# Kernel tuning notes

Measured on AMD Instinct MI355X. Metric: run time of the kernel, lower is better.

Reference implementation:

```python
import jax, jax.numpy as jnp
import numpy as np

B, L1, L2, C = 8, 2048, 2048, 320
H, D = 8, 64            # heads, dim_head -> inner_dim = 512
NREG = 4                # num_register_tokens
INNER = H * D
SCALE = D ** -0.5


def setup_inputs() -> dict:
    key = jax.random.key(0)
    ks = jax.random.split(key, 9)
    x = jax.random.normal(ks[0], (B, L1, C), dtype=jnp.float32)
    context = jax.random.normal(ks[1], (B, L2, C), dtype=jnp.float32)
    attn_mask = jax.random.randint(ks[2], (B, L1, L2), 0, 2).astype(bool)
    s = C ** -0.5
    Wq = jax.random.normal(ks[3], (C, INNER), dtype=jnp.float32) * s
    Wk = jax.random.normal(ks[4], (C, INNER), dtype=jnp.float32) * s
    Wv = jax.random.normal(ks[5], (C, INNER), dtype=jnp.float32) * s
    Wo = jax.random.normal(ks[6], (INNER, C), dtype=jnp.float32) * (INNER ** -0.5)
    bo = jnp.zeros((C,), dtype=jnp.float32)
    reg_tokens = jax.random.normal(ks[7], (1, NREG, C), dtype=jnp.float32)
    return {"x": x, "context": context, "attn_mask": attn_mask,
            "Wq": Wq, "Wk": Wk, "Wv": Wv, "Wo": Wo, "bo": bo,
            "reg_tokens": reg_tokens}


def reference(x, context, attn_mask, Wq, Wk, Wv, Wo, bo, reg_tokens):
    b = x.shape[0]
    # prepend register tokens to context: [B, NREG+L2, C]
    ctx = jnp.concatenate([jnp.broadcast_to(reg_tokens, (b, NREG, C)), context], axis=1)
    q = (x @ Wq).reshape(b, L1, H, D).transpose(0, 2, 1, 3)          # B H L1 D
    k = (ctx @ Wk).reshape(b, NREG + L2, H, D).transpose(0, 2, 1, 3)  # B H Lk D
    v = (ctx @ Wv).reshape(b, NREG + L2, H, D).transpose(0, 2, 1, 3)
    # pad mask with True for register tokens (always visible)
    mask = jnp.pad(attn_mask, ((0, 0), (0, 0), (NREG, 0)), constant_values=True)
    scores = jnp.einsum('bhqd,bhkd->bhqk', q, k) * SCALE              # B H L1 Lk
    scores = jnp.where(mask[:, None, :, :], scores, -jnp.inf)
    attn = jax.nn.softmax(scores, axis=-1)
    out = jnp.einsum('bhqk,bhkd->bhqd', attn, v)                      # B H L1 D
    out = out.transpose(0, 2, 1, 3).reshape(b, L1, INNER)             # B L1 (H D)
    return out @ Wo + bo
```

## Files before the change

kernel.cpp:

```cpp
#include <hip/hip_runtime.h>
#include <hip/hip_bf16.h>

#define B_ 8
#define L1_ 2048
#define L2_ 2048
#define C_ 320
#define H_ 8
#define D_ 64
#define NREG_ 4
#define INNER_ 512
#define LK_ 2052
#define LKP_ 2112
#define NKV_TILES 33
#define LOG2E 1.44269504f
#define QSCALE (0.125f * LOG2E)


typedef __bf16 bf16_t;
typedef __attribute__((ext_vector_type(8))) __bf16 bf16x8;
typedef __attribute__((ext_vector_type(4))) __bf16 bf16x4;
typedef __attribute__((ext_vector_type(4))) float f32x4;
typedef __attribute__((ext_vector_type(4))) unsigned int u32x4;

__device__ __forceinline__ f32x4 mfma16(bf16x8 a, bf16x8 b, f32x4 c){
  return __builtin_amdgcn_mfma_f32_16x16x32_bf16(a, b, c, 0, 0, 0);
}

__device__ __forceinline__ void gl_lds16(const char* g, char* l){
  __builtin_amdgcn_global_load_lds(
      (const __attribute__((address_space(1))) unsigned int*)g,
      (__attribute__((address_space(3))) unsigned int*)l, 16, 0, 0);
}

__device__ __forceinline__ float fexp2(float x){
  float r; asm("v_exp_f32 %0, %1" : "=v"(r) : "v"(x)); return r;
}

__device__ __forceinline__ unsigned cvtpk(float a, float b){
  unsigned r; asm("v_cvt_pk_bf16_f32 %0, %1, %2" : "=v"(r) : "v"(a), "v"(b)); return r;
}

__device__ __forceinline__ unsigned byte2bits(unsigned u){
  unsigned b = 0;
  b |= (u & 0x000000FFu) ? 1u : 0u;
  b |= (u & 0x0000FF00u) ? 2u : 0u;
  b |= (u & 0x00FF0000u) ? 4u : 0u;
  b |= (u & 0xFF000000u) ? 8u : 0u;
  return b;
}

__device__ __forceinline__ int swzK(int row){ return (row & 3) | ((row >> 1) & 4); }
__device__ __forceinline__ int swzV(int row){ return row & 7; }

__global__ __launch_bounds__(256)
void k_prep(const float* __restrict__ Wq, const float* __restrict__ Wk,
            const float* __restrict__ Wv, const float* __restrict__ Wo,
            bf16_t* __restrict__ Wqt, bf16_t* __restrict__ Wkt,
            bf16_t* __restrict__ Wvt, bf16_t* __restrict__ Wot,
            const float* __restrict__ x, const float* __restrict__ ctx,
            const float* __restrict__ regt,
            bf16_t* __restrict__ xb, bf16_t* __restrict__ ctxb,
            const void* __restrict__ maskv, unsigned int* __restrict__ maskp)
{
  int bid = blockIdx.x;
  int tid = threadIdx.x;
  if (bid < 1024){
    int z = bid >> 8, r = bid & 255, bx = r & 15, by = r >> 4;
    int K = (z < 3) ? C_ : INNER_;
    int N = (z < 3) ? INNER_ : C_;
    if (bx * 32 >= N || by * 32 >= K) return;
    const float* W = (z == 0) ? Wq : (z == 1) ? Wk : (z == 2) ? Wv : Wo;
    bf16_t* Wt = (z == 0) ? Wqt : (z == 1) ? Wkt : (z == 2) ? Wvt : Wot;
    float sc = (z == 0) ? QSCALE : 1.0f;
    __shared__ float t[32][33];
    int n0 = bx * 32, k0 = by * 32;
    int tx = tid & 31, ty = tid >> 5;
    for (int rr = ty; rr < 32; rr += 8) t[rr][tx] = W[(long)(k0 + rr) * N + n0 + tx];
    __syncthreads();
    for (int rr = ty; rr < 32; rr += 8) Wt[(long)(n0 + rr) * K + k0 + tx] = (bf16_t)(t[tx][rr] * sc);
  } else if (bid < 11424){
    int b2 = bid - 1024;
    if (b2 < 5120){
      long g = (long)b2 * 256 + tid;
      f32x4 v = *(const f32x4*)(x + g * 4);
      bf16x4 cv;
      cv[0]=(bf16_t)v[0]; cv[1]=(bf16_t)v[1]; cv[2]=(bf16_t)v[2]; cv[3]=(bf16_t)v[3];
      *(bf16x4*)(xb + g * 4) = cv;
    } else {
      long g = (long)(b2 - 5120) * 256 + tid;
      long row = g / 80;
      int col = (int)(g - row * 80) * 4;
      int b = (int)(row / LKP_);
      int rr = (int)(row - (long)b * LKP_);
      f32x4 v = (f32x4){0,0,0,0};
      if (rr < L2_)      v = *(const f32x4*)(ctx + ((long)(b * L1_ + rr)) * C_ + col);
      else if (rr < LK_) v = *(const f32x4*)(regt + (rr - L2_) * C_ + col);
      bf16x4 cv;
      cv[0]=(bf16_t)v[0]; cv[1]=(bf16_t)v[1]; cv[2]=(bf16_t)v[2]; cv[3]=(bf16_t)v[3];
      *(bf16x4*)(ctxb + row * C_ + col) = cv;
    }
  } else {
    int row = (bid - 11424) * 4 + (tid >> 6);
    int l = tid & 63;
    const unsigned char* mb = (const unsigned char*)maskv;
    const int* mi = (const int*)maskv;
    int bad = 0;
    #pragma unroll
    for (int jj = 0; jj < 4; jj++){
      int j = l + jj * 64;
      if ((j & 3) != 0 && mb[j] != 0) bad = 1;
    }
    int isInt = (__ballot(bad) == 0ull) ? 1 : 0;
    unsigned int* orow = maskp + (long)row * 66;
    if (!isInt){
      const unsigned char* rp = mb + (long)row * L2_;
      u32x4 a = *(const u32x4*)(rp + 32 * l);
      u32x4 c = *(const u32x4*)(rp + 32 * l + 16);
      unsigned wdv = 0;
      wdv |= byte2bits(a[0]);
      wdv |= byte2bits(a[1]) << 4;
      wdv |= byte2bits(a[2]) << 8;
      wdv |= byte2bits(a[3]) << 12;
      wdv |= byte2bits(c[0]) << 16;
      wdv |= byte2bits(c[1]) << 20;
      wdv |= byte2bits(c[2]) << 24;
      wdv |= byte2bits(c[3]) << 28;
      orow[l] = wdv;
      if (l == 0) orow[64] = 0x0000000Fu;
      else if (l == 1) orow[65] = 0u;
    } else {
      long base = (long)row * L2_;
      for (int s = 0; s < 33; s++){
        int kv = s * 64 + l;
        int vis;
        if (kv < L2_)      vis = (mi[base + kv] != 0);
        else               vis = (kv < LK_);
        unsigned long long bal = __ballot(vis);
        if (l == 0)      orow[2*s]   = (unsigned int)bal;
        else if (l == 1) orow[2*s+1] = (unsigned int)(bal >> 32);
      }
    }
  }
}

__global__ __launch_bounds__(256)
void k_proj(const bf16_t* __restrict__ xb, const bf16_t* __restrict__ ctxb,
            const bf16_t* __restrict__ Wqt, const bf16_t* __restrict__ Wkt,
            const bf16_t* __restrict__ Wvt,
            bf16_t* __restrict__ Qw, bf16_t* __restrict__ Kw, bf16_t* __restrict__ Vtw)
{
  int lin = blockIdx.x;
  int xcd = lin & 7, idx = lin >> 3;
  int mode, mt_, n_;
  if (idx < 64){
    mode = 0;
    mt_ = xcd * 16 + (idx & 15);
    n_ = idx >> 4;
  } else {
    int j = idx - 64;
    mode = 1 + (j & 1);
    int jj = j >> 1;
    n_ = jj & 3;
    int mm = jj >> 2;
    mt_ = mm * 8 + xcd;
    if (mt_ >= 132) return;
  }
  const char* Ab = (const char*)((mode == 0) ? xb : ctxb);
  const char* Wtb = (const char*)((mode == 0) ? Wqt : (mode == 1) ? Wkt : Wvt);
  bf16_t* out = (mode == 0) ? Qw : (mode == 1) ? Kw : Vtw;

  __shared__ __align__(16) char As[2][128*64*2];
  __shared__ __align__(16) char Bs[2][128*64*2];
  int tid = threadIdx.x;
  int w = tid >> 6, lane = tid & 63, cl = lane & 15, cg = lane >> 4;
  int wr = w >> 1, wc = w & 1;
  int m0 = mt_ * 128, n0 = n_ * 128;

  f32x4 acc[4][4];
  #pragma unroll
  for (int i = 0; i < 4; i++)
    #pragma unroll
    for (int j = 0; j < 4; j++) acc[i][j] = (f32x4){0,0,0,0};

  auto stage = [&](int kb, int buf){
    #pragma unroll
    for (int c = 0; c < 4; c++){
      int e = c * 4096 + tid * 16;
      int row = e >> 7, irb = e & 127;
      gl_lds16(Ab + (long)(m0 + row) * 640 + kb * 128 + (irb ^ ((row & 7) << 4)), As[buf] + e);
    }
    #pragma unroll
    for (int c = 0; c < 4; c++){
      int e = c * 4096 + tid * 16;
      int row = e >> 7, irb = e & 127;
      gl_lds16(Wtb + (long)(n0 + row) * 640 + kb * 128 + (irb ^ ((row & 7) << 4)), Bs[buf] + e);
    }
  };

  stage(0, 0);
  for (int kb = 0; kb < 5; ++kb){
    int buf = kb & 1;
    if (kb < 4){
      stage(kb + 1, buf ^ 1);
      asm volatile("s_waitcnt vmcnt(8)" ::: "memory");
    } else {
      asm volatile("s_waitcnt vmcnt(0)" ::: "memory");
    }
    __syncthreads();
    #pragma unroll
    for (int kc = 0; kc < 2; kc++){
      int kk = kc * 32 + cg * 8;
      bf16x8 af[4], bfr[4];
      #pragma unroll
      for (int mt = 0; mt < 4; mt++){
        int row = wr * 64 + mt * 16 + cl;
        af[mt] = *(const bf16x8*)(As[buf] + (row << 7) + ((kk << 1) ^ ((row & 7) << 4)));
      }
      #pragma unroll
      for (int nt = 0; nt < 4; nt++){
        int row = wc * 64 + nt * 16 + cl;
        bfr[nt] = *(const bf16x8*)(Bs[buf] + (row << 7) + ((kk << 1) ^ ((row & 7) << 4)));
      }
      #pragma unroll
      for (int mt = 0; mt < 4; mt++)
        #pragma unroll
        for (int nt = 0; nt < 4; nt++)
          acc[mt][nt] = mfma16(af[mt], bfr[nt], acc[mt][nt]);
    }
    __syncthreads();
  }

  #pragma unroll
  for (int mt = 0; mt < 4; mt++){
    #pragma unroll
    for (int nt = 0; nt < 4; nt++){
      f32x4 v = acc[mt][nt];
      int row = m0 + wr * 64 + mt * 16 + cg * 4;
      int col = n0 + wc * 64 + nt * 16 + cl;
      int h = col >> 6, d = col & 63;
      if (mode == 0){
        int b = row >> 11, l1 = row & 2047;
        bf16_t* p = out + ((long)((b * H_ + h) * L1_ + l1)) * D_ + d;
        #pragma unroll
        for (int r = 0; r < 4; r++) p[r * D_] = (bf16_t)v[r];
      } else if (mode == 1){
        int b = row / LKP_, rr = row - b * LKP_;
        bf16_t* p = out + ((long)((b * H_ + h) * LKP_ + rr)) * D_ + d;
        #pragma unroll
        for (int r = 0; r < 4; r++) p[r * D_] = (bf16_t)v[r];
      } else {
        int b = row / LKP_, rr = row - b * LKP_;
        bf16x4 cv;
        cv[0]=(bf16_t)v[0]; cv[1]=(bf16_t)v[1]; cv[2]=(bf16_t)v[2]; cv[3]=(bf16_t)v[3];
        *(bf16x4*)(out + ((long)((b * H_ + h) * D_ + d)) * LKP_ + rr) = cv;
      }
    }
  }
}

__global__ __launch_bounds__(512)
void k_attn(const bf16_t* __restrict__ Q, const bf16_t* __restrict__ K,
            const bf16_t* __restrict__ Vt, const unsigned int* __restrict__ maskp,
            bf16_t* __restrict__ att)
{
  __shared__ __align__(16) char smem[33024];
  int lin = blockIdx.x;
  int xcd = lin & 7, idx = lin >> 3;
  int bh = xcd * 8 + (idx >> 3);
  int qb = idx & 7;
  const int b = bh >> 3, h = bh & 7;
  const int tid = threadIdx.x, w = tid >> 6, lane = tid & 63;
  const int cl = lane & 15, cg = lane >> 4;
  const int qw = qb * 256 + w * 32;

  char* lutb = smem + 32768;
  if (tid < 16){
    unsigned n = tid;
    uint2 mk;
    mk.x = ((n & 1u) ? 0x0000FFFFu : 0u) | ((n & 2u) ? 0xFFFF0000u : 0u);
    mk.y = ((n & 4u) ? 0x0000FFFFu : 0u) | ((n & 8u) ? 0xFFFF0000u : 0u);
    *(uint2*)(lutb + tid * 8) = mk;
  }

  const char* Kg = (const char*)(K + (long)bh * LKP_ * D_);
  const char* Vg = (const char*)(Vt + (long)bh * D_ * LKP_);

  bf16x8 qf[2][2];
  const unsigned int* mrow[2];
  #pragma unroll
  for (int qg = 0; qg < 2; qg++){
    const bf16_t* Qb = Q + ((long)bh * L1_ + qw + qg*16 + cl) * D_;
    qf[qg][0] = *(const bf16x8*)(Qb + cg*8);
    qf[qg][1] = *(const bf16x8*)(Qb + 32 + cg*8);
    mrow[qg] = maskp + (long)(b * L1_ + qw + qg*16 + cl) * 66;
  }

  bf16x8 ones8;
  #pragma unroll
  for (int i = 0; i < 8; i++) ones8[i] = (bf16_t)1.0f;

  f32x4 o[2][4];
  f32x4 sacc[2];
  #pragma unroll
  for (int qg = 0; qg < 2; qg++){
    sacc[qg] = (f32x4){0,0,0,0};
    #pragma unroll
    for (int dt = 0; dt < 4; dt++) o[qg][dt] = (f32x4){0,0,0,0};
  }

  const int sp = tid * 16;
  const int srow = sp >> 7, sir = sp & 127;
  const int kgo = (srow << 7) + (sir ^ (swzK(srow) << 4));
  const long vgo = (long)srow * (LKP_ * 2) + (sir ^ (swzV(srow) << 4));

  gl_lds16(Kg + kgo, smem + sp);
  gl_lds16(Vg + vgo, smem + 16384 + sp);
  uint2 wd_cur[2];
  #pragma unroll
  for (int qg = 0; qg < 2; qg++) wd_cur[qg] = *(const uint2*)(mrow[qg]);
  asm volatile("s_waitcnt vmcnt(0)" ::: "memory");
  __syncthreads();

  for (int t = 0; t < NKV_TILES; ++t){
    int tn = (t + 1 < NKV_TILES) ? t + 1 : NKV_TILES - 1;
    gl_lds16(Kg + (long)tn * 8192 + kgo, smem + ((t + 1) & 1) * 8192 + sp);
    gl_lds16(Vg + vgo + tn * 128, smem + 16384 + ((t + 1) & 1) * 8192 + sp);
    uint2 wd_nxt[2];
    #pragma unroll
    for (int qg = 0; qg < 2; qg++) wd_nxt[qg] = *(const uint2*)(mrow[qg] + 2*tn);

    const char* Kb = smem + (t & 1) * 8192;
    const char* Vb = smem + 16384 + (t & 1) * 8192;

    f32x4 s[2][4];
    __builtin_amdgcn_s_setprio(1);
    #pragma unroll
    for (int T = 0; T < 4; T++){
      int row = 32*(T>>1) + 8*(cl>>2) + 4*(T&1) + (cl&3);
      int sw = swzK(row) << 4;
      const char* rp = Kb + (row << 7);
      bf16x8 kf0 = *(const bf16x8*)(rp + ((16*cg) ^ sw));
      bf16x8 kf1 = *(const bf16x8*)(rp + ((64 + 16*cg) ^ sw));
      #pragma unroll
      for (int qg = 0; qg < 2; qg++){
        f32x4 z = (f32x4){0,0,0,0};
        z = mfma16(kf0, qf[qg][0], z);
        z = mfma16(kf1, qf[qg][1], z);
        s[qg][T] = z;
      }
    }
    __builtin_amdgcn_s_setprio(0);

    bf16x8 pa[2][2];
    #pragma unroll
    for (int qg = 0; qg < 2; qg++){
      unsigned wrd[2][4];
      #pragma unroll
      for (int T = 0; T < 4; T++){
        unsigned wsel = (T < 2) ? wd_cur[qg].x : wd_cur[qg].y;
        unsigned nib = (wsel >> (8*cg + 4*(T&1))) & 0xFu;
        uint2 mk = *(const uint2*)(lutb + (nib << 3));
        float p0 = fexp2(s[qg][T][0]);
        float p1 = fexp2(s[qg][T][1]);
        float p2 = fexp2(s[qg][T][2]);
        float p3 = fexp2(s[qg][T][3]);
        unsigned lo = cvtpk(p0, p1) & mk.x;
        unsigned hi = cvtpk(p2, p3) & mk.y;
        wrd[T >> 1][2*(T & 1) + 0] = lo;
        wrd[T >> 1][2*(T & 1) + 1] = hi;
      }
      union { u32x4 u; bf16x8 v; } pk0, pk1;
      pk0.u = (u32x4){wrd[0][0], wrd[0][1], wrd[0][2], wrd[0][3]};
      pk1.u = (u32x4){wrd[1][0], wrd[1][1], wrd[1][2], wrd[1][3]};
      pa[qg][0] = pk0.v;
      pa[qg][1] = pk1.v;
    }

    __builtin_amdgcn_s_setprio(1);
    #pragma unroll
    for (int qg = 0; qg < 2; qg++){
      sacc[qg] = mfma16(ones8, pa[qg][0], sacc[qg]);
      sacc[qg] = mfma16(ones8, pa[qg][1], sacc[qg]);
    }
    #pragma unroll
    for (int dt = 0; dt < 4; dt++){
      int row = 16*dt + cl;
      int sw = swzV(row) << 4;
      const char* rp = Vb + (row << 7);
      bf16x8 vf0 = *(const bf16x8*)(rp + ((16*cg) ^ sw));
      bf16x8 vf1 = *(const bf16x8*)(rp + ((64 + 16*cg) ^ sw));
      #pragma unroll
      for (int qg = 0; qg < 2; qg++){
        o[qg][dt] = mfma16(pa[qg][0], vf0, o[qg][dt]);
        o[qg][dt] = mfma16(pa[qg][1], vf1, o[qg][dt]);
      }
    }
    __builtin_amdgcn_s_setprio(0);

    asm volatile("s_waitcnt vmcnt(0)" ::: "memory");
    __syncthreads();
    wd_cur[0] = wd_nxt[0];
    wd_cur[1] = wd_nxt[1];
  }

  #pragma unroll
  for (int qg = 0; qg < 2; qg++){
    float inv = 1.0f / sacc[qg][0];
    float ir0 = __shfl(inv, (lane & 48) | (cg*4 + 0));
    float ir1 = __shfl(inv, (lane & 48) | (cg*4 + 1));
    float ir2 = __shfl(inv, (lane & 48) | (cg*4 + 2));
    float ir3 = __shfl(inv, (lane & 48) | (cg*4 + 3));
    int qbase = qw + qg*16 + cg*4;
    #pragma unroll
    for (int dt = 0; dt < 4; dt++){
      bf16_t* op = att + ((long)(b * L1_) + qbase) * INNER_ + h * D_ + 16*dt + cl;
      op[0] = (bf16_t)(o[qg][dt][0] * ir0);
      op[INNER_] = (bf16_t)(o[qg][dt][1] * ir1);
      op[2*INNER_] = (bf16_t)(o[qg][dt][2] * ir2);
      op[3*INNER_] = (bf16_t)(o[qg][dt][3] * ir3);
    }
  }
}

__global__ __launch_bounds__(256)
void k_out(const bf16_t* __restrict__ A, const bf16_t* __restrict__ Wot,
           const float* __restrict__ bo, float* __restrict__ out)
{
  __shared__ __align__(16) char As[2][128*64*2];
  __shared__ __align__(16) char Bs[2][64*64*2];
  int lin = blockIdx.x;
  int xcd = lin & 7, idx = lin >> 3;
  int tid = threadIdx.x;
  int w = tid >> 6, lane = tid & 63, cl = lane & 15, cg = lane >> 4;
  int wr = w >> 1, wc = w & 1;
  int m0 = (xcd * 16 + (idx & 15)) * 128, n0 = (idx >> 4) * 64;
  const char* Ab = (const char*)A;
  const char* Bb = (const char*)Wot;

  f32x4 acc[4][2];
  #pragma unroll
  for (int i = 0; i < 4; i++)
    #pragma unroll
    for (int j = 0; j < 2; j++) acc[i][j] = (f32x4){0,0,0,0};

  auto stage = [&](int kb, int buf){
    #pragma unroll
    for (int c = 0; c < 4; c++){
      int e = c * 4096 + tid * 16;
      int row = e >> 7, irb = e & 127;
      gl_lds16(Ab + (long)(m0 + row) * 1024 + kb * 128 + (irb ^ ((row & 7) << 4)), As[buf] + e);
    }
    #pragma unroll
    for (int c = 0; c < 2; c++){
      int e = c * 4096 + tid * 16;
      int row = e >> 7, irb = e & 127;
      gl_lds16(Bb + (long)(n0 + row) * 1024 + kb * 128 + (irb ^ ((row & 7) << 4)), Bs[buf] + e);
    }
  };

  stage(0, 0);
  for (int kb = 0; kb < 8; kb++){
    int buf = kb & 1;
    if (kb < 7){
      stage(kb + 1, buf ^ 1);
      asm volatile("s_waitcnt vmcnt(6)" ::: "memory");
    } else {
      asm volatile("s_waitcnt vmcnt(0)" ::: "memory");
    }
    __syncthreads();
    #pragma unroll
    for (int kc = 0; kc < 2; kc++){
      int kk = kc * 32 + cg * 8;
      bf16x8 af[4], bfr[2];
      #pragma unroll
      for (int mt = 0; mt < 4; mt++){
        int row = wr * 64 + mt * 16 + cl;
        af[mt] = *(const bf16x8*)(As[buf] + (row << 7) + ((kk << 1) ^ ((row & 7) << 4)));
      }
      #pragma unroll
      for (int nt = 0; nt < 2; nt++){
        int row = wc * 32 + nt * 16 + cl;
        bfr[nt] = *(const bf16x8*)(Bs[buf] + (row << 7) + ((kk << 1) ^ ((row & 7) << 4)));
      }
      #pragma unroll
      for (int mt = 0; mt < 4; mt++)
        #pragma unroll
        for (int nt = 0; nt < 2; nt++)
          acc[mt][nt] = mfma16(af[mt], bfr[nt], acc[mt][nt]);
    }
    __syncthreads();
  }
  #pragma unroll
  for (int mt = 0; mt < 4; mt++)
    #pragma unroll
    for (int nt = 0; nt < 2; nt++){
      int row = m0 + wr * 64 + mt * 16 + cg * 4;
      int col = n0 + wc * 32 + nt * 16 + cl;
      float bias = bo[col];
      #pragma unroll
      for (int r = 0; r < 4; r++)
        out[(long)(row + r) * C_ + col] = acc[mt][nt][r] + bias;
    }
}

extern "C" void kernel_launch(void* const* d_in, const int* in_sizes, int n_in,
                              void* d_out, int out_size, void* d_ws, size_t ws_size,
                              hipStream_t stream)
{
  const float* x    = (const float*)d_in[0];
  const float* ctx  = (const float*)d_in[1];
  const void*  mask = d_in[2];
  const float* Wq   = (const float*)d_in[3];
  const float* Wk   = (const float*)d_in[4];
  const float* Wv   = (const float*)d_in[5];
  const float* Wo   = (const float*)d_in[6];
  const float* bo   = (const float*)d_in[7];
  const float* regt = (const float*)d_in[8];
  float* out = (float*)d_out;

  char* ws = (char*)d_ws;
  size_t off = 256;
  unsigned int* maskp = (unsigned int*)(ws + off);    off += (size_t)16384 * 66 * 4;
  bf16_t* Qw  = (bf16_t*)(ws + off);                  off += (size_t)B_*H_*L1_*D_*2;
  bf16_t* Kw  = (bf16_t*)(ws + off);                  off += (size_t)B_*H_*LKP_*D_*2;
  bf16_t* Vtw = (bf16_t*)(ws + off);                  off += (size_t)B_*H_*D_*LKP_*2;
  size_t Roff = off;
  bf16_t* xb   = (bf16_t*)(ws + Roff);
  bf16_t* ctxb = (bf16_t*)(ws + Roff + (size_t)16384*C_*2);
  bf16_t* Att  = (bf16_t*)(ws + Roff);
  off = Roff + (size_t)16384*C_*2 + (size_t)16896*C_*2;
  bf16_t* Wqt = (bf16_t*)(ws + off);                  off += (size_t)C_*INNER_*2;
  bf16_t* Wkt = (bf16_t*)(ws + off);                  off += (size_t)C_*INNER_*2;
  bf16_t* Wvt = (bf16_t*)(ws + off);                  off += (size_t)C_*INNER_*2;
  bf16_t* Wot = (bf16_t*)(ws + off);                  off += (size_t)C_*INNER_*2;
  (void)ws_size; (void)in_sizes; (void)n_in; (void)out_size;

  k_prep<<<15520, 256, 0, stream>>>(Wq, Wk, Wv, Wo, Wqt, Wkt, Wvt, Wot,
                                    x, ctx, regt, xb, ctxb, mask, maskp);
  k_proj<<<1600, 256, 0, stream>>>(xb, ctxb, Wqt, Wkt, Wvt, Qw, Kw, Vtw);
  k_attn<<<512, 512, 0, stream>>>(Qw, Kw, Vtw, maskp, Att);
  k_out<<<640, 256, 0, stream>>>(Att, Wot, bo, out);
}
```

Measured before the change: 179.7 us.

## Move mask bit-packing into projection kernel and widen bf16 conversion stores

Mask bit-packing moves out of the prep kernel and into the projection GEMM kernel. Each projection block runs its GEMM tile (or skips it if out of range) and then packs a grid-strided share of mask rows, so the mask traffic overlaps with the matmul work. The fp32-to-bf16 conversion of x and context now handles two float4 groups per thread with packed conversions and 16-byte stores, which shrinks the prep grid. The risk is that the mask work lengthens some projection blocks and adds tail imbalance, since 1600 blocks cover 4096 row groups unevenly.

```diff
diff --git a/kernel.cpp b/kernel.cpp
--- a/kernel.cpp
+++ b/kernel.cpp
@@ -59,8 +59,7 @@
             bf16_t* __restrict__ Wvt, bf16_t* __restrict__ Wot,
             const float* __restrict__ x, const float* __restrict__ ctx,
             const float* __restrict__ regt,
-            bf16_t* __restrict__ xb, bf16_t* __restrict__ ctxb,
-            const void* __restrict__ maskv, unsigned int* __restrict__ maskp)
+            bf16_t* __restrict__ xb, bf16_t* __restrict__ ctxb)
 {
   int bid = blockIdx.x;
   int tid = threadIdx.x;
@@ -78,16 +77,20 @@
     for (int rr = ty; rr < 32; rr += 8) t[rr][tx] = W[(long)(k0 + rr) * N + n0 + tx];
     __syncthreads();
     for (int rr = ty; rr < 32; rr += 8) Wt[(long)(n0 + rr) * K + k0 + tx] = (bf16_t)(t[tx][rr] * sc);
-  } else if (bid < 11424){
-    int b2 = bid - 1024;
-    if (b2 < 5120){
-      long g = (long)b2 * 256 + tid;
-      f32x4 v = *(const f32x4*)(x + g * 4);
-      bf16x4 cv;
-      cv[0]=(bf16_t)v[0]; cv[1]=(bf16_t)v[1]; cv[2]=(bf16_t)v[2]; cv[3]=(bf16_t)v[3];
-      *(bf16x4*)(xb + g * 4) = cv;
-    } else {
-      long g = (long)(b2 - 5120) * 256 + tid;
+  } else if (bid < 3584){
+    long g0 = ((long)(bid - 1024) * 256 + tid) * 2;
+    f32x4 v0 = *(const f32x4*)(x + g0 * 4);
+    f32x4 v1 = *(const f32x4*)(x + g0 * 4 + 4);
+    union { u32x4 u; bf16x8 v; } pk;
+    pk.u = (u32x4){cvtpk(v0[0], v0[1]), cvtpk(v0[2], v0[3]),
+                   cvtpk(v1[0], v1[1]), cvtpk(v1[2], v1[3])};
+    *(bf16x8*)(xb + g0 * 4) = pk.v;
+  } else {
+    long g0 = ((long)(bid - 3584) * 256 + tid) * 2;
+    f32x4 vv[2];
+    #pragma unroll
+    for (int gg = 0; gg < 2; gg++){
+      long g = g0 + gg;
       long row = g / 80;
       int col = (int)(g - row * 80) * 4;
       int b = (int)(row / LKP_);
@@ -95,51 +98,12 @@
       f32x4 v = (f32x4){0,0,0,0};
       if (rr < L2_)      v = *(const f32x4*)(ctx + ((long)(b * L1_ + rr)) * C_ + col);
       else if (rr < LK_) v = *(const f32x4*)(regt + (rr - L2_) * C_ + col);
-      bf16x4 cv;
-      cv[0]=(bf16_t)v[0]; cv[1]=(bf16_t)v[1]; cv[2]=(bf16_t)v[2]; cv[3]=(bf16_t)v[3];
-      *(bf16x4*)(ctxb + row * C_ + col) = cv;
-    }
-  } else {
-    int row = (bid - 11424) * 4 + (tid >> 6);
-    int l = tid & 63;
-    const unsigned char* mb = (const unsigned char*)maskv;
-    const int* mi = (const int*)maskv;
-    int bad = 0;
-    #pragma unroll
-    for (int jj = 0; jj < 4; jj++){
-      int j = l + jj * 64;
-      if ((j & 3) != 0 && mb[j] != 0) bad = 1;
-    }
-    int isInt = (__ballot(bad) == 0ull) ? 1 : 0;
-    unsigned int* orow = maskp + (long)row * 66;
-    if (!isInt){
-      const unsigned char* rp = mb + (long)row * L2_;
-      u32x4 a = *(const u32x4*)(rp + 32 * l);
-      u32x4 c = *(const u32x4*)(rp + 32 * l + 16);
-      unsigned wdv = 0;
-      wdv |= byte2bits(a[0]);
-      wdv |= byte2bits(a[1]) << 4;
-      wdv |= byte2bits(a[2]) << 8;
-      wdv |= byte2bits(a[3]) << 12;
-      wdv |= byte2bits(c[0]) << 16;
-      wdv |= byte2bits(c[1]) << 20;
-      wdv |= byte2bits(c[2]) << 24;
-      wdv |= byte2bits(c[3]) << 28;
-      orow[l] = wdv;
-      if (l == 0) orow[64] = 0x0000000Fu;
-      else if (l == 1) orow[65] = 0u;
-    } else {
-      long base = (long)row * L2_;
-      for (int s = 0; s < 33; s++){
-        int kv = s * 64 + l;
-        int vis;
-        if (kv < L2_)      vis = (mi[base + kv] != 0);
-        else               vis = (kv < LK_);
-        unsigned long long bal = __ballot(vis);
-        if (l == 0)      orow[2*s]   = (unsigned int)bal;
-        else if (l == 1) orow[2*s+1] = (unsigned int)(bal >> 32);
-      }
-    }
+      vv[gg] = v;
+    }
+    union { u32x4 u; bf16x8 v; } pk;
+    pk.u = (u32x4){cvtpk(vv[0][0], vv[0][1]), cvtpk(vv[0][2], vv[0][3]),
+                   cvtpk(vv[1][0], vv[1][1]), cvtpk(vv[1][2], vv[1][3])};
+    *(bf16x8*)(ctxb + g0 * 4) = pk.v;
   }
 }
 
@@ -147,7 +111,8 @@
 void k_proj(const bf16_t* __restrict__ xb, const bf16_t* __restrict__ ctxb,
             const bf16_t* __restrict__ Wqt, const bf16_t* __restrict__ Wkt,
             const bf16_t* __restrict__ Wvt,
-            bf16_t* __restrict__ Qw, bf16_t* __restrict__ Kw, bf16_t* __restrict__ Vtw)
+            bf16_t* __restrict__ Qw, bf16_t* __restrict__ Kw, bf16_t* __restrict__ Vtw,
+            const void* __restrict__ maskv, unsigned int* __restrict__ maskp)
 {
   int lin = blockIdx.x;
   int xcd = lin & 7, idx = lin >> 3;
@@ -163,96 +128,144 @@
     n_ = jj & 3;
     int mm = jj >> 2;
     mt_ = mm * 8 + xcd;
-    if (mt_ >= 132) return;
-  }
-  const char* Ab = (const char*)((mode == 0) ? xb : ctxb);
-  const char* Wtb = (const char*)((mode == 0) ? Wqt : (mode == 1) ? Wkt : Wvt);
-  bf16_t* out = (mode == 0) ? Qw : (mode == 1) ? Kw : Vtw;
-
-  __shared__ __align__(16) char As[2][128*64*2];
-  __shared__ __align__(16) char Bs[2][128*64*2];
+  }
   int tid = threadIdx.x;
-  int w = tid >> 6, lane = tid & 63, cl = lane & 15, cg = lane >> 4;
-  int wr = w >> 1, wc = w & 1;
-  int m0 = mt_ * 128, n0 = n_ * 128;
-
-  f32x4 acc[4][4];
-  #pragma unroll
-  for (int i = 0; i < 4; i++)
-    #pragma unroll
-    for (int j = 0; j < 4; j++) acc[i][j] = (f32x4){0,0,0,0};
-
-  auto stage = [&](int kb, int buf){
-    #pragma unroll
-    for (int c = 0; c < 4; c++){
-      int e = c * 4096 + tid * 16;
-      int row = e >> 7, irb = e & 127;
-      gl_lds16(Ab + (long)(m0 + row) * 640 + kb * 128 + (irb ^ ((row & 7) << 4)), As[buf] + e);
-    }
-    #pragma unroll
-    for (int c = 0; c < 4; c++){
-      int e = c * 4096 + tid * 16;
-      int row = e >> 7, irb = e & 127;
-      gl_lds16(Wtb + (long)(n0 + row) * 640 + kb * 128 + (irb ^ ((row & 7) << 4)), Bs[buf] + e);
-    }
-  };
-
-  stage(0, 0);
-  for (int kb = 0; kb < 5; ++kb){
-    int buf = kb & 1;
-    if (kb < 4){
-      stage(kb + 1, buf ^ 1);
-      asm volatile("s_waitcnt vmcnt(8)" ::: "memory");
-    } else {
-      asm volatile("s_waitcnt vmcnt(0)" ::: "memory");
-    }
-    __syncthreads();
-    #pragma unroll
-    for (int kc = 0; kc < 2; kc++){
-      int kk = kc * 32 + cg * 8;
-      bf16x8 af[4], bfr[4];
-      #pragma unroll
-      for (int mt = 0; mt < 4; mt++){
-        int row = wr * 64 + mt * 16 + cl;
-        af[mt] = *(const bf16x8*)(As[buf] + (row << 7) + ((kk << 1) ^ ((row & 7) << 4)));
-      }
+  bool valid = (mode == 0) || (mt_ < 132);
+
+  if (valid){
+    const char* Ab = (const char*)((mode == 0) ? xb : ctxb);
+    const char* Wtb = (const char*)((mode == 0) ? Wqt : (mode == 1) ? Wkt : Wvt);
+    bf16_t* out = (mode == 0) ? Qw : (mode == 1) ? Kw : Vtw;
+
+    __shared__ __align__(16) char As[2][128*64*2];
+    __shared__ __align__(16) char Bs[2][128*64*2];
+    int w = tid >> 6, lane = tid & 63, cl = lane & 15, cg = lane >> 4;
+    int wr = w >> 1, wc = w & 1;
+    int m0 = mt_ * 128, n0 = n_ * 128;
+
+    f32x4 acc[4][4];
+    #pragma unroll
+    for (int i = 0; i < 4; i++)
+      #pragma unroll
+      for (int j = 0; j < 4; j++) acc[i][j] = (f32x4){0,0,0,0};
+
+    auto stage = [&](int kb, int buf){
+      #pragma unroll
+      for (int c = 0; c < 4; c++){
+        int e = c * 4096 + tid * 16;
+        int row = e >> 7, irb = e & 127;
+        gl_lds16(Ab + (long)(m0 + row) * 640 + kb * 128 + (irb ^ ((row & 7) << 4)), As[buf] + e);
+      }
+      #pragma unroll
+      for (int c = 0; c < 4; c++){
+        int e = c * 4096 + tid * 16;
+        int row = e >> 7, irb = e & 127;
+        gl_lds16(Wtb + (long)(n0 + row) * 640 + kb * 128 + (irb ^ ((row & 7) << 4)), Bs[buf] + e);
+      }
+    };
+
+    stage(0, 0);
+    for (int kb = 0; kb < 5; ++kb){
+      int buf = kb & 1;
+      if (kb < 4){
+        stage(kb + 1, buf ^ 1);
+        asm volatile("s_waitcnt vmcnt(8)" ::: "memory");
+      } else {
+        asm volatile("s_waitcnt vmcnt(0)" ::: "memory");
+      }
+      __syncthreads();
+      #pragma unroll
+      for (int kc = 0; kc < 2; kc++){
+        int kk = kc * 32 + cg * 8;
+        bf16x8 af[4], bfr[4];
+        #pragma unroll
+        for (int mt = 0; mt < 4; mt++){
+          int row = wr * 64 + mt * 16 + cl;
+          af[mt] = *(const bf16x8*)(As[buf] + (row << 7) + ((kk << 1) ^ ((row & 7) << 4)));
+        }
+        #pragma unroll
+        for (int nt = 0; nt < 4; nt++){
+          int row = wc * 64 + nt * 16 + cl;
+          bfr[nt] = *(const bf16x8*)(Bs[buf] + (row << 7) + ((kk << 1) ^ ((row & 7) << 4)));
+        }
+        #pragma unroll
+        for (int mt = 0; mt < 4; mt++)
+          #pragma unroll
+          for (int nt = 0; nt < 4; nt++)
+            acc[mt][nt] = mfma16(af[mt], bfr[nt], acc[mt][nt]);
+      }
+      __syncthreads();
+    }
+
+    #pragma unroll
+    for (int mt = 0; mt < 4; mt++){
       #pragma unroll
       for (int nt = 0; nt < 4; nt++){
-        int row = wc * 64 + nt * 16 + cl;
-        bfr[nt] = *(const bf16x8*)(Bs[buf] + (row << 7) + ((kk << 1) ^ ((row & 7) << 4)));
-      }
-      #pragma unroll
-      for (int mt = 0; mt < 4; mt++)
-        #pragma unroll
-        for (int nt = 0; nt < 4; nt++)
-          acc[mt][nt] = mfma16(af[mt], bfr[nt], acc[mt][nt]);
-    }
-    __syncthreads();
-  }
-
-  #pragma unroll
-  for (int mt = 0; mt < 4; mt++){
-    #pragma unroll
-    for (int nt = 0; nt < 4; nt++){
-      f32x4 v = acc[mt][nt];
-      int row = m0 + wr * 64 + mt * 16 + cg * 4;
-      int col = n0 + wc * 64 + nt * 16 + cl;
-      int h = col >> 6, d = col & 63;
-      if (mode == 0){
-        int b = row >> 11, l1 = row & 2047;
-        bf16_t* p = out + ((long)((b * H_ + h) * L1_ + l1)) * D_ + d;
-        #pragma unroll
-        for (int r = 0; r < 4; r++) p[r * D_] = (bf16_t)v[r];
-      } else if (mode == 1){
-        int b = row / LKP_, rr = row - b * LKP_;
-        bf16_t* p = out + ((long)((b * H_ + h) * LKP_ + rr)) * D_ + d;
-        #pragma unroll
-        for (int r = 0; r < 4; r++) p[r * D_] = (bf16_t)v[r];
+        f32x4 v = acc[mt][nt];
+        int row = m0 + wr * 64 + mt * 16 + cg * 4;
+        int col = n0 + wc * 64 + nt * 16 + cl;
+        int h = col >> 6, d = col & 63;
+        if (mode == 0){
+          int b = row >> 11, l1 = row & 2047;
+          bf16_t* p = out + ((long)((b * H_ + h) * L1_ + l1)) * D_ + d;
+          #pragma unroll
+          for (int r = 0; r < 4; r++) p[r * D_] = (bf16_t)v[r];
+        } else if (mode == 1){
+          int b = row / LKP_, rr = row - b * LKP_;
+          bf16_t* p = out + ((long)((b * H_ + h) * LKP_ + rr)) * D_ + d;
+          #pragma unroll
+          for (int r = 0; r < 4; r++) p[r * D_] = (bf16_t)v[r];
+        } else {
+          int b = row / LKP_, rr = row - b * LKP_;
+          bf16x4 cv;
+          cv[0]=(bf16_t)v[0]; cv[1]=(bf16_t)v[1]; cv[2]=(bf16_t)v[2]; cv[3]=(bf16_t)v[3];
+          *(bf16x4*)(out + ((long)((b * H_ + h) * D_ + d)) * LKP_ + rr) = cv;
+        }
+      }
+    }
+  }
+
+  {
+    int l = tid & 63;
+    const unsigned char* mb = (const unsigned char*)maskv;
+    const int* mi = (const int*)maskv;
+    int bad = 0;
+    #pragma unroll
+    for (int jj = 0; jj < 4; jj++){
+      int j = l + jj * 64;
+      if ((j & 3) != 0 && mb[j] != 0) bad = 1;
+    }
+    int isInt = (__ballot(bad) == 0ull) ? 1 : 0;
+    for (int mq = lin; mq < 4096; mq += 1600){
+      int row = mq * 4 + (tid >> 6);
+      unsigned int* orow = maskp + (long)row * 66;
+      if (!isInt){
+        const unsigned char* rp = mb + (long)row * L2_;
+        u32x4 a = *(const u32x4*)(rp + 32 * l);
+        u32x4 c = *(const u32x4*)(rp + 32 * l + 16);
+        unsigned wdv = 0;
+        wdv |= byte2bits(a[0]);
+        wdv |= byte2bits(a[1]) << 4;
+        wdv |= byte2bits(a[2]) << 8;
+        wdv |= byte2bits(a[3]) << 12;
+        wdv |= byte2bits(c[0]) << 16;
+        wdv |= byte2bits(c[1]) << 20;
+        wdv |= byte2bits(c[2]) << 24;
+        wdv |= byte2bits(c[3]) << 28;
+        orow[l] = wdv;
+        if (l == 0) orow[64] = 0x0000000Fu;
+        else if (l == 1) orow[65] = 0u;
       } else {
-        int b = row / LKP_, rr = row - b * LKP_;
-        bf16x4 cv;
-        cv[0]=(bf16_t)v[0]; cv[1]=(bf16_t)v[1]; cv[2]=(bf16_t)v[2]; cv[3]=(bf16_t)v[3];
-        *(bf16x4*)(out + ((long)((b * H_ + h) * D_ + d)) * LKP_ + rr) = cv;
+        long base = (long)row * L2_;
+        for (int s = 0; s < 33; s++){
+          int kv = s * 64 + l;
+          int vis;
+          if (kv < L2_) vis = (mi[base + kv] != 0);
+          else          vis = (kv < LK_);
+          unsigned long long bal = __ballot(vis);
+          if (l == 0)      orow[2*s]   = (unsigned int)bal;
+          else if (l == 1) orow[2*s+1] = (unsigned int)(bal >> 32);
+        }
       }
     }
   }
@@ -535,9 +548,9 @@
   bf16_t* Wot = (bf16_t*)(ws + off);                  off += (size_t)C_*INNER_*2;
   (void)ws_size; (void)in_sizes; (void)n_in; (void)out_size;
 
-  k_prep<<<15520, 256, 0, stream>>>(Wq, Wk, Wv, Wo, Wqt, Wkt, Wvt, Wot,
-                                    x, ctx, regt, xb, ctxb, mask, maskp);
-  k_proj<<<1600, 256, 0, stream>>>(xb, ctxb, Wqt, Wkt, Wvt, Qw, Kw, Vtw);
+  k_prep<<<6224, 256, 0, stream>>>(Wq, Wk, Wv, Wo, Wqt, Wkt, Wvt, Wot,
+                                   x, ctx, regt, xb, ctxb);
+  k_proj<<<1600, 256, 0, stream>>>(xb, ctxb, Wqt, Wkt, Wvt, Qw, Kw, Vtw, mask, maskp);
   k_attn<<<512, 512, 0, stream>>>(Qw, Kw, Vtw, maskp, Att);
   k_out<<<640, 256, 0, stream>>>(Att, Wot, bo, out);
 }
```

Result: slower. 270.1 us (+50.3%).

## Fuse fp32-to-bf16 input conversion into projection GEMM operand loads

Applied to the files above, without the earlier changes.

Drops the separate conversion of x and context (plus register tokens) to bf16 from the prep kernel. The projection kernel now reads fp32 activations directly, converts them in registers and writes them into swizzled LDS. This removes a full write and re-read of the bf16 activation copies. In exchange, the projection GEMM loses its double-buffered async pipeline: it becomes single-buffered with synchronous loads, which exposes memory latency. The A-operand global traffic inside the GEMM also doubles because it reads fp32.

```diff
diff --git a/kernel.cpp b/kernel.cpp
--- a/kernel.cpp
+++ b/kernel.cpp
@@ -57,9 +57,6 @@
             const float* __restrict__ Wv, const float* __restrict__ Wo,
             bf16_t* __restrict__ Wqt, bf16_t* __restrict__ Wkt,
             bf16_t* __restrict__ Wvt, bf16_t* __restrict__ Wot,
-            const float* __restrict__ x, const float* __restrict__ ctx,
-            const float* __restrict__ regt,
-            bf16_t* __restrict__ xb, bf16_t* __restrict__ ctxb,
             const void* __restrict__ maskv, unsigned int* __restrict__ maskp)
 {
   int bid = blockIdx.x;
@@ -78,29 +75,8 @@
     for (int rr = ty; rr < 32; rr += 8) t[rr][tx] = W[(long)(k0 + rr) * N + n0 + tx];
     __syncthreads();
     for (int rr = ty; rr < 32; rr += 8) Wt[(long)(n0 + rr) * K + k0 + tx] = (bf16_t)(t[tx][rr] * sc);
-  } else if (bid < 11424){
-    int b2 = bid - 1024;
-    if (b2 < 5120){
-      long g = (long)b2 * 256 + tid;
-      f32x4 v = *(const f32x4*)(x + g * 4);
-      bf16x4 cv;
-      cv[0]=(bf16_t)v[0]; cv[1]=(bf16_t)v[1]; cv[2]=(bf16_t)v[2]; cv[3]=(bf16_t)v[3];
-      *(bf16x4*)(xb + g * 4) = cv;
-    } else {
-      long g = (long)(b2 - 5120) * 256 + tid;
-      long row = g / 80;
-      int col = (int)(g - row * 80) * 4;
-      int b = (int)(row / LKP_);
-      int rr = (int)(row - (long)b * LKP_);
-      f32x4 v = (f32x4){0,0,0,0};
-      if (rr < L2_)      v = *(const f32x4*)(ctx + ((long)(b * L1_ + rr)) * C_ + col);
-      else if (rr < LK_) v = *(const f32x4*)(regt + (rr - L2_) * C_ + col);
-      bf16x4 cv;
-      cv[0]=(bf16_t)v[0]; cv[1]=(bf16_t)v[1]; cv[2]=(bf16_t)v[2]; cv[3]=(bf16_t)v[3];
-      *(bf16x4*)(ctxb + row * C_ + col) = cv;
-    }
   } else {
-    int row = (bid - 11424) * 4 + (tid >> 6);
+    int row = (bid - 1024) * 4 + (tid >> 6);
     int l = tid & 63;
     const unsigned char* mb = (const unsigned char*)maskv;
     const int* mi = (const int*)maskv;
@@ -133,8 +109,8 @@
       for (int s = 0; s < 33; s++){
         int kv = s * 64 + l;
         int vis;
-        if (kv < L2_)      vis = (mi[base + kv] != 0);
-        else               vis = (kv < LK_);
+        if (kv < L2_) vis = (mi[base + kv] != 0);
+        else          vis = (kv < LK_);
         unsigned long long bal = __ballot(vis);
         if (l == 0)      orow[2*s]   = (unsigned int)bal;
         else if (l == 1) orow[2*s+1] = (unsigned int)(bal >> 32);
@@ -144,7 +120,8 @@
 }
 
 __global__ __launch_bounds__(256)
-void k_proj(const bf16_t* __restrict__ xb, const bf16_t* __restrict__ ctxb,
+void k_proj(const float* __restrict__ x, const float* __restrict__ ctx,
+            const float* __restrict__ regt,
             const bf16_t* __restrict__ Wqt, const bf16_t* __restrict__ Wkt,
             const bf16_t* __restrict__ Wvt,
             bf16_t* __restrict__ Qw, bf16_t* __restrict__ Kw, bf16_t* __restrict__ Vtw)
@@ -165,47 +142,63 @@
     mt_ = mm * 8 + xcd;
     if (mt_ >= 132) return;
   }
-  const char* Ab = (const char*)((mode == 0) ? xb : ctxb);
-  const char* Wtb = (const char*)((mode == 0) ? Wqt : (mode == 1) ? Wkt : Wvt);
+  const bf16_t* Wt = (mode == 0) ? Wqt : (mode == 1) ? Wkt : Wvt;
+  const char* Wtb = (const char*)Wt;
   bf16_t* out = (mode == 0) ? Qw : (mode == 1) ? Kw : Vtw;
 
-  __shared__ __align__(16) char As[2][128*64*2];
-  __shared__ __align__(16) char Bs[2][128*64*2];
+  __shared__ __align__(16) char As[128*64*2];
+  __shared__ __align__(16) char Bs[128*64*2];
   int tid = threadIdx.x;
   int w = tid >> 6, lane = tid & 63, cl = lane & 15, cg = lane >> 4;
   int wr = w >> 1, wc = w & 1;
   int m0 = mt_ * 128, n0 = n_ * 128;
 
+  const float* srcs[8];
+  #pragma unroll
+  for (int c = 0; c < 8; c++){
+    int e = c * 1024 + tid * 4;
+    int row = e >> 6, k = e & 63;
+    if (mode == 0){
+      srcs[c] = x + (long)(m0 + row) * C_ + k;
+    } else {
+      int rg = m0 + row;
+      int b = rg / LKP_;
+      int rr = rg - b * LKP_;
+      const float* src = nullptr;
+      if (rr < L2_)      src = ctx + (long)(b * L1_ + rr) * C_ + k;
+      else if (rr < LK_) src = regt + (long)(rr - L2_) * C_ + k;
+      srcs[c] = src;
+    }
+  }
+
   f32x4 acc[4][4];
   #pragma unroll
   for (int i = 0; i < 4; i++)
     #pragma unroll
     for (int j = 0; j < 4; j++) acc[i][j] = (f32x4){0,0,0,0};
 
-  auto stage = [&](int kb, int buf){
+  for (int kb = 0; kb < 5; ++kb){
+    int k0 = kb * 64;
+    __syncthreads();
     #pragma unroll
     for (int c = 0; c < 4; c++){
       int e = c * 4096 + tid * 16;
       int row = e >> 7, irb = e & 127;
-      gl_lds16(Ab + (long)(m0 + row) * 640 + kb * 128 + (irb ^ ((row & 7) << 4)), As[buf] + e);
-    }
-    #pragma unroll
-    for (int c = 0; c < 4; c++){
-      int e = c * 4096 + tid * 16;
-      int row = e >> 7, irb = e & 127;
-      gl_lds16(Wtb + (long)(n0 + row) * 640 + kb * 128 + (irb ^ ((row & 7) << 4)), Bs[buf] + e);
-    }
-  };
-
-  stage(0, 0);
-  for (int kb = 0; kb < 5; ++kb){
-    int buf = kb & 1;
-    if (kb < 4){
-      stage(kb + 1, buf ^ 1);
-      asm volatile("s_waitcnt vmcnt(8)" ::: "memory");
-    } else {
-      asm volatile("s_waitcnt vmcnt(0)" ::: "memory");
-    }
+      gl_lds16(Wtb + (long)(n0 + row) * 640 + kb * 128 + (irb ^ ((row & 7) << 4)), Bs + e);
+    }
+    #pragma unroll
+    for (int c = 0; c < 8; c++){
+      int e = c * 1024 + tid * 4;
+      int row = e >> 6, k = e & 63;
+      f32x4 v = (f32x4){0,0,0,0};
+      if (srcs[c]) v = *(const f32x4*)(srcs[c] + k0);
+      uint2 pk;
+      pk.x = cvtpk(v[0], v[1]);
+      pk.y = cvtpk(v[2], v[3]);
+      int off = (row << 7) + ((k << 1) ^ ((row & 7) << 4));
+      *(uint2*)(As + off) = pk;
+    }
+    asm volatile("s_waitcnt vmcnt(0)" ::: "memory");
     __syncthreads();
     #pragma unroll
     for (int kc = 0; kc < 2; kc++){
@@ -214,12 +207,12 @@
       #pragma unroll
       for (int mt = 0; mt < 4; mt++){
         int row = wr * 64 + mt * 16 + cl;
-        af[mt] = *(const bf16x8*)(As[buf] + (row << 7) + ((kk << 1) ^ ((row & 7) << 4)));
+        af[mt] = *(const bf16x8*)(As + (row << 7) + ((kk << 1) ^ ((row & 7) << 4)));
       }
       #pragma unroll
       for (int nt = 0; nt < 4; nt++){
         int row = wc * 64 + nt * 16 + cl;
-        bfr[nt] = *(const bf16x8*)(Bs[buf] + (row << 7) + ((kk << 1) ^ ((row & 7) << 4)));
+        bfr[nt] = *(const bf16x8*)(Bs + (row << 7) + ((kk << 1) ^ ((row & 7) << 4)));
       }
       #pragma unroll
       for (int mt = 0; mt < 4; mt++)
@@ -227,7 +220,6 @@
         for (int nt = 0; nt < 4; nt++)
           acc[mt][nt] = mfma16(af[mt], bfr[nt], acc[mt][nt]);
     }
-    __syncthreads();
   }
 
   #pragma unroll
@@ -524,20 +516,15 @@
   bf16_t* Qw  = (bf16_t*)(ws + off);                  off += (size_t)B_*H_*L1_*D_*2;
   bf16_t* Kw  = (bf16_t*)(ws + off);                  off += (size_t)B_*H_*LKP_*D_*2;
   bf16_t* Vtw = (bf16_t*)(ws + off);                  off += (size_t)B_*H_*D_*LKP_*2;
-  size_t Roff = off;
-  bf16_t* xb   = (bf16_t*)(ws + Roff);
-  bf16_t* ctxb = (bf16_t*)(ws + Roff + (size_t)16384*C_*2);
-  bf16_t* Att  = (bf16_t*)(ws + Roff);
-  off = Roff + (size_t)16384*C_*2 + (size_t)16896*C_*2;
+  bf16_t* Att = (bf16_t*)(ws + off);                  off += (size_t)B_*L1_*INNER_*2;
   bf16_t* Wqt = (bf16_t*)(ws + off);                  off += (size_t)C_*INNER_*2;
   bf16_t* Wkt = (bf16_t*)(ws + off);                  off += (size_t)C_*INNER_*2;
   bf16_t* Wvt = (bf16_t*)(ws + off);                  off += (size_t)C_*INNER_*2;
   bf16_t* Wot = (bf16_t*)(ws + off);                  off += (size_t)C_*INNER_*2;
   (void)ws_size; (void)in_sizes; (void)n_in; (void)out_size;
 
-  k_prep<<<15520, 256, 0, stream>>>(Wq, Wk, Wv, Wo, Wqt, Wkt, Wvt, Wot,
-                                    x, ctx, regt, xb, ctxb, mask, maskp);
-  k_proj<<<1600, 256, 0, stream>>>(xb, ctxb, Wqt, Wkt, Wvt, Qw, Kw, Vtw);
+  k_prep<<<5120, 256, 0, stream>>>(Wq, Wk, Wv, Wo, Wqt, Wkt, Wvt, Wot, mask, maskp);
+  k_proj<<<1600, 256, 0, stream>>>(x, ctx, regt, Wqt, Wkt, Wvt, Qw, Kw, Vtw);
   k_attn<<<512, 512, 0, stream>>>(Qw, Kw, Vtw, maskp, Att);
   k_out<<<640, 256, 0, stream>>>(Att, Wot, bo, out);
 }
```

Result: slower. 223.3 us (+24.2%).
